# Kernel optimization log

Measured on AMD Instinct MI355X. Metric: run time of the kernel, lower is better.

Reference implementation:

```python
import jax, jax.numpy as jnp
import numpy as np

N_AGENTS = 8; N_HEADS = 4; HYP = 128; EMB = 32; ENT_DIM = 64
BS = 64; T = 64; NE = 32


def setup_inputs() -> dict:
    key = jax.random.key(0)
    ks = jax.random.split(key, 8)
    p = lambda k, shape: jax.random.normal(k, shape, dtype=jnp.float32) * 0.1
    return {
        "agent_qs": jax.random.normal(ks[0], (BS, T, N_AGENTS), dtype=jnp.float32),
        "entities": jax.random.normal(ks[1], (BS, T, NE, ENT_DIM), dtype=jnp.float32),
        "entity_mask": jax.random.randint(ks[2], (BS, T, NE), 0, 2, dtype=jnp.int32),
        "fc1_w": p(ks[3], (4, HYP, ENT_DIM)), "fc1_b": jnp.zeros((4, HYP), jnp.float32),
        "qkv_w": p(ks[4], (4, 3 * HYP, HYP)), "qkv_b": jnp.zeros((4, 3 * HYP), jnp.float32),
        "out_w": p(ks[5], (4, HYP, HYP)), "out_b": jnp.zeros((4, HYP), jnp.float32),
        "fc2_w": p(ks[6], (4, EMB, HYP)), "fc2_b": jnp.zeros((4, EMB), jnp.float32),
    }


def _hypernet(entities, emask, fc1_w, fc1_b, qkv_w, qkv_b, out_w, out_b, fc2_w, fc2_b):
    # entities: [B, ne, ed]; emask: [B, ne] int (1 = entity absent)
    B, ne, _ = entities.shape
    hd = HYP // N_HEADS
    x1 = jax.nn.relu(jnp.einsum('bne,he->bnh', entities, fc1_w) + fc1_b)  # [B, ne, HYP]
    agent_mask = emask[:, :N_AGENTS]                                      # [B, na]
    # attn_mask = 1 - (1-agent_mask) x (1-entity_mask); nonzero => masked out
    attn_mask = 1.0 - (1.0 - agent_mask.astype(jnp.float32))[:, :, None] * \
                      (1.0 - emask.astype(jnp.float32))[:, None, :]       # [B, na, ne]
    qkv = jnp.einsum('bnh,gh->bng', x1, qkv_w) + qkv_b                    # [B, ne, 3*HYP]
    q, k, v = jnp.split(qkv, 3, axis=-1)
    q = q[:, :N_AGENTS].reshape(B, N_AGENTS, N_HEADS, hd).transpose(0, 2, 1, 3)
    k = k.reshape(B, ne, N_HEADS, hd).transpose(0, 2, 1, 3)
    v = v.reshape(B, ne, N_HEADS, hd).transpose(0, 2, 1, 3)
    logits = jnp.einsum('bhqd,bhkd->bhqk', q, k) / jnp.sqrt(jnp.float32(hd))
    masked = attn_mask[:, None] > 0                                       # [B, 1, na, ne]
    logits = jnp.where(masked, -1e9, logits)
    w = jax.nn.softmax(logits, axis=-1)
    # rows fully masked -> zero weights (matches nan-fill in torch impl)
    w = jnp.where(jnp.all(masked, axis=-1, keepdims=True), 0.0, w)
    attn = jnp.einsum('bhqk,bhkd->bhqd', w, v).transpose(0, 2, 1, 3).reshape(B, N_AGENTS, HYP)
    x2 = jnp.einsum('bnh,oh->bno', attn, out_w) + out_b
    x2 = jnp.where(agent_mask[:, :, None] > 0, 0.0, x2)                   # post_mask
    x3 = jnp.einsum('bnh,eh->bne', x2, fc2_w) + fc2_b
    x3 = jnp.where(agent_mask[:, :, None] > 0, 0.0, x3)                   # masked_fill
    return x3  # [B, n_agents, EMB]


def reference(agent_qs, entities, entity_mask, fc1_w, fc1_b, qkv_w, qkv_b, out_w, out_b, fc2_w, fc2_b):
    bs, t, ne, ed = entities.shape
    ents = entities.reshape(bs * t, ne, ed)
    emask = entity_mask.reshape(bs * t, ne)
    qs = agent_qs.reshape(bs * t, 1, N_AGENTS)
    # vmap over the 4 stacked hypernets (w1, b1, w_final, V)
    outs = jax.vmap(_hypernet, in_axes=(None, None, 0, 0, 0, 0, 0, 0, 0, 0))(
        ents, emask, fc1_w, fc1_b, qkv_w, qkv_b, out_w, out_b, fc2_w, fc2_b)
    w1 = jax.nn.softmax(outs[0], axis=-1)            # matrix mode: [B, na, EMB]
    b1 = outs[1].mean(axis=1)[:, None, :]            # vector mode: [B, 1, EMB]
    wf = outs[2].mean(axis=1)[:, :, None]            # vector mode: [B, EMB, 1]
    wf = jax.nn.softmax(wf, axis=-1)                 # softmax over size-1 dim (faithful)
    v = outs[3].mean(axis=(1, 2))[:, None, None]     # scalar mode: [B, 1, 1]
    hidden = jnp.einsum('bqa,bae->bqe', qs, w1) + b1
    y = jnp.einsum('bqe,bek->bqk', hidden, wf) + v
    return y.reshape(bs, t, 1)
```

## Files before the change

### kernel.cpp

```cpp
#include <hip/hip_runtime.h>
#include <math.h>

#define BPB 4
#define NBLK 1024

typedef short short8 __attribute__((ext_vector_type(8)));
typedef float f32x4 __attribute__((ext_vector_type(4)));

__device__ __forceinline__ unsigned short f2bf(float x) {
  unsigned int u = __float_as_uint(x);
  u += 0x7fffu + ((u >> 16) & 1u);
  return (unsigned short)(u >> 16);
}
__device__ __forceinline__ float bf2f(unsigned int lo16) {
  return __uint_as_float(lo16 << 16);
}
__device__ __forceinline__ int tile_addr(int r, int k) {
  int g = k >> 3;
  int p = (g ^ ((r >> 1) & 3)) & 3;
  return r * 32 + p * 8 + (k & 7);
}
__device__ __forceinline__ int rm_addr(int r, int k) {
  int g = k >> 3;
  int r3 = r & 7;
  int rot = ((r3 << 2) | (r3 >> 1)) & 7;
  int p = (g & 8) | ((g & 7) ^ rot);
  return r * 128 + p * 8 + (k & 7);
}

__global__ void prep_w(const float* __restrict__ fc1_w, const float* __restrict__ qkv_w,
                       unsigned short* __restrict__ wbf) {
  int gid = blockIdx.x * 256 + threadIdx.x;
  for (int o = gid * 2; o < gid * 2 + 2; ++o) {
    float v; int dst;
    if (o < 16384) {
      int gi = o >> 13, rem = o & 8191, n = rem >> 6, k = rem & 63;
      int g = gi ? 3 : 1;
      v = fc1_w[((g << 7) + n) * 64 + k];
      dst = gi * 40960 + ((n >> 4) * 2 + (k >> 5)) * 512 + tile_addr(n & 15, k & 31);
    } else if (o < 49152) {
      int o2 = o - 16384;
      int gi = o2 >> 14, rem = o2 & 16383, n = rem >> 7, k = rem & 127;
      int g = gi ? 3 : 1;
      v = qkv_w[((g * 384 + 128 + n) << 7) + k];
      dst = gi * 40960 + 8192 + ((n >> 4) * 4 + (k >> 5)) * 512 + tile_addr(n & 15, k & 31);
    } else {
      int o2 = o - 49152;
      int gi = o2 >> 14, rem = o2 & 16383, n = rem >> 7, k = rem & 127;
      int g = gi ? 3 : 1;
      v = qkv_w[((g * 384 + n) << 7) + k];
      dst = gi * 40960 + 24576 + ((n >> 4) * 4 + (k >> 5)) * 512 + tile_addr(n & 15, k & 31);
    }
    wbf[dst] = f2bf(v);
  }
}

__global__ void prep_misc(const float* __restrict__ qkv_w, const float* __restrict__ qkv_b,
                          const float* __restrict__ out_w, const float* __restrict__ out_b,
                          const float* __restrict__ fc2_w, const float* __restrict__ fc2_b,
                          float* __restrict__ wsf) {
  const int gslot = blockIdx.x;
  const int g = gslot ? 3 : 1;
  const int t = threadIdx.x;
  __shared__ float cw[128];
  __shared__ float ow2[128];
  if (t < 128) {
    const float* fw = fc2_w + g * 32 * 128;
    float s = 0.f;
    for (int e = 0; e < 32; ++e) s += fw[e * 128 + t];
    cw[t] = s;
  }
  __syncthreads();
  if (t < 128) {
    const float* ow = out_w + g * 128 * 128;
    float s = 0.f;
    for (int h = 0; h < 128; ++h) s += ow[h * 128 + t] * cw[h];
    ow2[t] = s;
  }
  __syncthreads();
  float* wsg = wsf + gslot * 1024;
  const float* qwv = qkv_w + (size_t)(g * 3 + 2) * 128 * 128;
  for (int o = t; o < 512; o += 256) {
    int hh = o >> 7, h2 = o & 127;
    float s = 0.f;
    for (int d = 0; d < 32; ++d) s += qwv[(hh * 32 + d) * 128 + h2] * ow2[hh * 32 + d];
    wsg[o] = s;
  }
  if (t < 4) {
    const float* qbv = qkv_b + g * 384 + 256;
    float s = 0.f;
    for (int d = 0; d < 32; ++d) s += qbv[t * 32 + d] * ow2[t * 32 + d];
    wsg[512 + t] = s;
  }
  if (t == 0) {
    const float* ob = out_b + g * 128;
    float oc = 0.f;
    for (int h = 0; h < 128; ++h) oc += ob[h] * cw[h];
    const float* fb = fc2_b + g * 32;
    float cb = 0.f;
    for (int e = 0; e < 32; ++e) cb += fb[e];
    wsg[516] = oc + cb;
  }
}

__global__ __launch_bounds__(512, 1)
void mixer(const float* __restrict__ agent_qs,
           const float* __restrict__ entities,
           const int* __restrict__ emask,
           const float* __restrict__ fc1_b,
           const float* __restrict__ qkv_b,
           const unsigned short* __restrict__ wbf,
           const float* __restrict__ wsf,
           float* __restrict__ out) {
  __shared__ __align__(16) unsigned short sW[24576];
  __shared__ __align__(16) unsigned short sEK[16384];
  __shared__ __align__(16) unsigned short sX1[16384];
  __shared__ __align__(16) unsigned short sQ[4096];
  __shared__ __align__(16) float sVW[1024];
  __shared__ float sVP[BPB][4][32];
  __shared__ int sMm[BPB * 32];
  __shared__ float sS[8];

  const int t = threadIdx.x;
  const int lane = t & 63;
  const int w = t >> 6;
  const int bb0 = blockIdx.x * BPB;

  if (t < BPB * 32) sMm[t] = emask[bb0 * 32 + t];

  float wreg[4][2][4];

  for (int gi = 0; gi < 2; ++gi) {
    const int g = gi ? 3 : 1;
    __syncthreads();
    {
      const uint4* src = (const uint4*)(wbf + gi * 40960);
      uint4* dst = (uint4*)sW;
#pragma unroll
      for (int i = 0; i < 6; ++i) dst[i * 512 + t] = src[i * 512 + t];
      if (t < 256) ((float4*)sVW)[t] = ((const float4*)(wsf + gi * 1024))[t];
      const float4* Eg = (const float4*)(entities) + (size_t)bb0 * 512;
#pragma unroll
      for (int i = 0; i < 4; ++i) {
        int f4 = i * 512 + t;
        float4 v = Eg[f4];
        int k4 = f4 & 15, e = (f4 >> 4) & 31, bbi = f4 >> 9;
        int k = k4 * 4;
        int addr = bbi * 2048 + ((e >> 4) * 2 + (k >> 5)) * 512 + tile_addr(e & 15, k & 31);
        uint2 pk;
        pk.x = (unsigned)f2bf(v.x) | ((unsigned)f2bf(v.y) << 16);
        pk.y = (unsigned)f2bf(v.z) | ((unsigned)f2bf(v.w) << 16);
        *(uint2*)&sEK[addr] = pk;
      }
    }
    __syncthreads();
    {
      const int b = w >> 1, mtl = w & 1;
      const int r = lane & 15, kg = lane >> 4;
      f32x4 acc[8];
#pragma unroll
      for (int nt = 0; nt < 8; ++nt) acc[nt] = {0.f, 0.f, 0.f, 0.f};
#pragma unroll
      for (int kc = 0; kc < 2; ++kc) {
        short8 af = *(const short8*)&sEK[b * 2048 + (mtl * 2 + kc) * 512 + tile_addr(r, kg * 8)];
#pragma unroll
        for (int nt = 0; nt < 8; ++nt) {
          short8 bf = *(const short8*)&sW[(nt * 2 + kc) * 512 + tile_addr(r, kg * 8)];
          acc[nt] = __builtin_amdgcn_mfma_f32_16x16x32_bf16(af, bf, acc[nt], 0, 0, 0);
        }
      }
      const float* b1 = fc1_b + g * 128;
#pragma unroll
      for (int nt = 0; nt < 8; ++nt) {
        int h = nt * 16 + r;
        float bias = b1[h];
        int kc = h >> 5;
#pragma unroll
        for (int reg = 0; reg < 4; ++reg) {
          int rr = kg * 4 + reg;
          float v = acc[nt][reg] + bias;
          v = v > 0.f ? v : 0.f;
          sX1[b * 4096 + (mtl * 4 + kc) * 512 + tile_addr(rr, h & 31)] = f2bf(v);
        }
      }
    }
    __syncthreads();
    {
      const int b = w >> 1, mtl = w & 1;
      const int r = lane & 15, kg = lane >> 4;
      f32x4 acc[8];
#pragma unroll
      for (int nt = 0; nt < 8; ++nt) acc[nt] = {0.f, 0.f, 0.f, 0.f};
#pragma unroll
      for (int kc = 0; kc < 4; ++kc) {
        short8 af = *(const short8*)&sX1[b * 4096 + (mtl * 4 + kc) * 512 + tile_addr(r, kg * 8)];
#pragma unroll
        for (int nt = 0; nt < 8; ++nt) {
          short8 bf = *(const short8*)&sW[8192 + (nt * 4 + kc) * 512 + tile_addr(r, kg * 8)];
          acc[nt] = __builtin_amdgcn_mfma_f32_16x16x32_bf16(af, bf, acc[nt], 0, 0, 0);
        }
      }
      const float* bk = qkv_b + g * 384 + 128;
#pragma unroll
      for (int nt = 0; nt < 8; ++nt) {
        int h = nt * 16 + r;
        float bias = bk[h];
#pragma unroll
        for (int reg = 0; reg < 4; ++reg) {
          int ent = mtl * 16 + kg * 4 + reg;
          sEK[b * 4096 + rm_addr(ent, h)] = f2bf(acc[nt][reg] + bias);
        }
      }
    }
    __syncthreads();
    {
      const uint4* src = (const uint4*)(wbf + gi * 40960 + 24576);
      uint4* dst = (uint4*)(sW + 8192);
#pragma unroll
      for (int i = 0; i < 4; ++i) dst[i * 512 + t] = src[i * 512 + t];
    }
    __syncthreads();
    {
      const int mt = w >> 2;
      const int r = lane & 15, kg = lane >> 4;
      const int b_rd = mt * 2 + (r >> 3);
      f32x4 acc[2];
      acc[0] = {0.f, 0.f, 0.f, 0.f};
      acc[1] = {0.f, 0.f, 0.f, 0.f};
#pragma unroll
      for (int kc = 0; kc < 4; ++kc) {
        short8 af = *(const short8*)&sX1[b_rd * 4096 + kc * 512 + tile_addr(r & 7, kg * 8)];
#pragma unroll
        for (int j = 0; j < 2; ++j) {
          int nt = (w & 3) * 2 + j;
          short8 bf = *(const short8*)&sW[8192 + (nt * 4 + kc) * 512 + tile_addr(r, kg * 8)];
          acc[j] = __builtin_amdgcn_mfma_f32_16x16x32_bf16(af, bf, acc[j], 0, 0, 0);
        }
      }
      const float* bq = qkv_b + g * 384;
#pragma unroll
      for (int j = 0; j < 2; ++j) {
        int nt = (w & 3) * 2 + j;
        int h = nt * 16 + r;
        float bias = bq[h];
#pragma unroll
        for (int reg = 0; reg < 4; ++reg) {
          int rr = kg * 4 + reg;
          int b_st = mt * 2 + (rr >> 3);
          sQ[b_st * 1024 + rm_addr(rr & 7, h)] = f2bf(acc[j][reg] + bias);
        }
      }
    }
    __syncthreads();
    if (w < 4) {
      const int b = w;
      const int cl = lane & 15, kg = lane >> 4;
      bool ea0 = (sMm[b * 32 + cl] == 0);
      bool ea1 = (sMm[b * 32 + 16 + cl] == 0);
      bool aa[4];
#pragma unroll
      for (int reg = 0; reg < 4; ++reg) aa[reg] = (sMm[b * 32 + ((kg * 4 + reg) & 7)] == 0);
#pragma unroll
      for (int hh = 0; hh < 4; ++hh) {
        short8 af = *(const short8*)&sQ[b * 1024 + rm_addr(lane & 7, hh * 32 + kg * 8)];
        f32x4 d[2];
#pragma unroll
        for (int nt = 0; nt < 2; ++nt) {
          f32x4 z = {0.f, 0.f, 0.f, 0.f};
          short8 bf = *(const short8*)&sEK[b * 4096 + rm_addr(nt * 16 + cl, hh * 32 + kg * 8)];
          d[nt] = __builtin_amdgcn_mfma_f32_16x16x32_bf16(af, bf, z, 0, 0, 0);
        }
#pragma unroll
        for (int reg = 0; reg < 4; ++reg) {
          float lg0 = (ea0 && aa[reg]) ? d[0][reg] * 0.17677669529663687f : -1e30f;
          float lg1 = (ea1 && aa[reg]) ? d[1][reg] * 0.17677669529663687f : -1e30f;
          float m = fmaxf(lg0, lg1);
          for (int o = 8; o; o >>= 1) m = fmaxf(m, __shfl_xor(m, o, 16));
          float p0 = lg0 > -1e29f ? __expf(lg0 - m) : 0.f;
          float p1 = lg1 > -1e29f ? __expf(lg1 - m) : 0.f;
          float s = p0 + p1;
          for (int o = 8; o; o >>= 1) s += __shfl_xor(s, o, 16);
          float inv = s > 0.f ? 1.f / s : 0.f;
          wreg[hh][0][reg] = p0 * inv;
          wreg[hh][1][reg] = p1 * inv;
        }
      }
    } else {
      const int b = w - 4;
      const int e = lane & 31;
      const int hh0 = (lane >> 5) * 2;
      const int mt = e >> 4, r = e & 15;
      float a0 = sVW[512 + hh0];
      float a1 = sVW[512 + hh0 + 1];
#pragma unroll
      for (int kc = 0; kc < 4; ++kc) {
#pragma unroll
        for (int gg = 0; gg < 4; ++gg) {
          uint4 u = *(const uint4*)&sX1[b * 4096 + (mt * 4 + kc) * 512 + tile_addr(r, gg * 8)];
          int kb = kc * 32 + gg * 8;
          const float* w0 = &sVW[hh0 * 128 + kb];
          const float* w1 = &sVW[(hh0 + 1) * 128 + kb];
          float x0 = bf2f(u.x & 0xffffu), x1v = bf2f(u.x >> 16);
          float x2 = bf2f(u.y & 0xffffu), x3v = bf2f(u.y >> 16);
          float x4 = bf2f(u.z & 0xffffu), x5v = bf2f(u.z >> 16);
          float x6 = bf2f(u.w & 0xffffu), x7v = bf2f(u.w >> 16);
          a0 = fmaf(x0, w0[0], a0); a0 = fmaf(x1v, w0[1], a0);
          a0 = fmaf(x2, w0[2], a0); a0 = fmaf(x3v, w0[3], a0);
          a0 = fmaf(x4, w0[4], a0); a0 = fmaf(x5v, w0[5], a0);
          a0 = fmaf(x6, w0[6], a0); a0 = fmaf(x7v, w0[7], a0);
          a1 = fmaf(x0, w1[0], a1); a1 = fmaf(x1v, w1[1], a1);
          a1 = fmaf(x2, w1[2], a1); a1 = fmaf(x3v, w1[3], a1);
          a1 = fmaf(x4, w1[4], a1); a1 = fmaf(x5v, w1[5], a1);
          a1 = fmaf(x6, w1[6], a1); a1 = fmaf(x7v, w1[7], a1);
        }
      }
      sVP[b][hh0][e] = a0;
      sVP[b][hh0 + 1][e] = a1;
    }
    __syncthreads();
    if (w < 4) {
      const int b = w;
      const int cl = lane & 15;
      float c = 0.f;
#pragma unroll
      for (int hh = 0; hh < 4; ++hh) {
        float vp0 = sVP[b][hh][cl];
        float vp1 = sVP[b][hh][16 + cl];
        float s0 = wreg[hh][0][0] + wreg[hh][0][1] + wreg[hh][0][2] + wreg[hh][0][3];
        float s1 = wreg[hh][1][0] + wreg[hh][1][1] + wreg[hh][1][2] + wreg[hh][1][3];
        c = fmaf(vp0, s0, fmaf(vp1, s1, c));
      }
      for (int o = 16; o; o >>= 1) c += __shfl_xor(c, o, 32);
      if (lane == 0) {
        int cnt = 0;
        for (int a = 0; a < 8; ++a) cnt += (sMm[b * 32 + a] == 0);
        sS[gi * 4 + b] = c + sVW[516] * (float)cnt;
      }
    }
  }
  __syncthreads();
  if (t < BPB) {
    const float* qs = agent_qs + (size_t)(bb0 + t) * 8;
    float q = 0.f;
    for (int a = 0; a < 8; ++a) q += qs[a];
    out[bb0 + t] = q + sS[t] * 0.125f + sS[4 + t] * (1.f / 256.f);
  }
}

extern "C" void kernel_launch(void* const* d_in, const int* in_sizes, int n_in,
                              void* d_out, int out_size, void* d_ws, size_t ws_size,
                              hipStream_t stream) {
  const float* agent_qs = (const float*)d_in[0];
  const float* entities = (const float*)d_in[1];
  const int* emask = (const int*)d_in[2];
  const float* fc1_w = (const float*)d_in[3];
  const float* fc1_b = (const float*)d_in[4];
  const float* qkv_w = (const float*)d_in[5];
  const float* qkv_b = (const float*)d_in[6];
  const float* out_w = (const float*)d_in[7];
  const float* out_b = (const float*)d_in[8];
  const float* fc2_w = (const float*)d_in[9];
  const float* fc2_b = (const float*)d_in[10];
  float* out = (float*)d_out;
  unsigned short* wbf = (unsigned short*)d_ws;
  float* wsf = (float*)((char*)d_ws + 163840);

  prep_w<<<160, 256, 0, stream>>>(fc1_w, qkv_w, wbf);
  prep_misc<<<2, 256, 0, stream>>>(qkv_w, qkv_b, out_w, out_b, fc2_w, fc2_b, wsf);
  mixer<<<NBLK, 512, 0, stream>>>(agent_qs, entities, emask, fc1_b, qkv_b, wbf, wsf, out);
}
```

Before: 169.3 us.

## Read MFMA weight fragments directly from global memory and drop the shared weight staging

Weights are now pre-packed by a single merged prep kernel into per-lane MFMA fragment order, so each lane loads its B operand straight from global memory (L2-resident) instead of first copying weights into a 48KB shared buffer. This removes the sW staging copies and several barriers, merges the Q projection and V-projection work into the K-projection phase, and raises launch bounds so more blocks can share a CU. Epilogue stores are vectorised into packed bf16 pairs. The cost is repeated global/L2 traffic for the weights across blocks, with higher register pressure from the larger occupancy target.

Measured after the change: 174.6 us. 3.1% more time.

```diff
diff --git a/kernel.cpp b/kernel.cpp
--- a/kernel.cpp
+++ b/kernel.cpp
@@ -3,6 +3,7 @@
 
 #define BPB 4
 #define NBLK 1024
+#define SCALE 0.17677669529663687f
 
 typedef short short8 __attribute__((ext_vector_type(8)));
 typedef float f32x4 __attribute__((ext_vector_type(4)));
@@ -11,6 +12,9 @@
   unsigned int u = __float_as_uint(x);
   u += 0x7fffu + ((u >> 16) & 1u);
   return (unsigned short)(u >> 16);
+}
+__device__ __forceinline__ unsigned pk2(float a, float b) {
+  return (unsigned)f2bf(a) | ((unsigned)f2bf(b) << 16);
 }
 __device__ __forceinline__ float bf2f(unsigned int lo16) {
   return __uint_as_float(lo16 << 16);
@@ -28,82 +32,94 @@
   return r * 128 + p * 8 + (k & 7);
 }
 
-__global__ void prep_w(const float* __restrict__ fc1_w, const float* __restrict__ qkv_w,
-                       unsigned short* __restrict__ wbf) {
-  int gid = blockIdx.x * 256 + threadIdx.x;
-  for (int o = gid * 2; o < gid * 2 + 2; ++o) {
-    float v; int dst;
-    if (o < 16384) {
-      int gi = o >> 13, rem = o & 8191, n = rem >> 6, k = rem & 63;
+__global__ void prep(const float* __restrict__ fc1_w, const float* __restrict__ qkv_w,
+                     const float* __restrict__ qkv_b, const float* __restrict__ out_w,
+                     const float* __restrict__ out_b, const float* __restrict__ fc2_w,
+                     const float* __restrict__ fc2_b,
+                     unsigned short* __restrict__ wbf, float* __restrict__ wsf) {
+  const int blk = blockIdx.x;
+  const int t = threadIdx.x;
+  __shared__ float cw[128], ow2[128], red[128];
+  if (blk < 40) {
+    int o = blk * 256 + t;
+    const float* src;
+    int dst;
+    if (o < 2048) {
+      int gi = o >> 10, rem = o & 1023, n = rem >> 3, kg = rem & 7;
       int g = gi ? 3 : 1;
-      v = fc1_w[((g << 7) + n) * 64 + k];
-      dst = gi * 40960 + ((n >> 4) * 2 + (k >> 5)) * 512 + tile_addr(n & 15, k & 31);
-    } else if (o < 49152) {
-      int o2 = o - 16384;
-      int gi = o2 >> 14, rem = o2 & 16383, n = rem >> 7, k = rem & 127;
+      src = fc1_w + ((g << 7) + n) * 64 + kg * 8;
+      int lane = (kg & 3) * 16 + (n & 15);
+      int f = (n >> 4) * 2 + (kg >> 2);
+      dst = ((gi * 16 + f) * 64 + lane) * 8;
+    } else if (o < 6144) {
+      int o2 = o - 2048;
+      int gi = o2 >> 11, rem = o2 & 2047, n = rem >> 4, kg = rem & 15;
       int g = gi ? 3 : 1;
-      v = qkv_w[((g * 384 + 128 + n) << 7) + k];
-      dst = gi * 40960 + 8192 + ((n >> 4) * 4 + (k >> 5)) * 512 + tile_addr(n & 15, k & 31);
+      src = qkv_w + ((g * 384 + 128 + n) << 7) + kg * 8;
+      int lane = (kg & 3) * 16 + (n & 15);
+      int f = (n >> 4) * 4 + (kg >> 2);
+      dst = 16384 + ((gi * 32 + f) * 64 + lane) * 8;
     } else {
-      int o2 = o - 49152;
-      int gi = o2 >> 14, rem = o2 & 16383, n = rem >> 7, k = rem & 127;
+      int o2 = o - 6144;
+      int gi = o2 >> 11, rem = o2 & 2047, n = rem >> 4, kg = rem & 15;
       int g = gi ? 3 : 1;
-      v = qkv_w[((g * 384 + n) << 7) + k];
-      dst = gi * 40960 + 24576 + ((n >> 4) * 4 + (k >> 5)) * 512 + tile_addr(n & 15, k & 31);
-    }
-    wbf[dst] = f2bf(v);
+      src = qkv_w + ((g * 384 + n) << 7) + kg * 8;
+      int lane = (kg & 3) * 16 + (n & 15);
+      int f = (n >> 4) * 4 + (kg >> 2);
+      dst = 49152 + ((gi * 32 + f) * 64 + lane) * 8;
+    }
+    float4 v0 = *(const float4*)src;
+    float4 v1 = *(const float4*)(src + 4);
+    uint4 p;
+    p.x = pk2(v0.x, v0.y); p.y = pk2(v0.z, v0.w);
+    p.z = pk2(v1.x, v1.y); p.w = pk2(v1.z, v1.w);
+    *(uint4*)&wbf[dst] = p;
+  } else {
+    const int gi = blk - 40;
+    const int g = gi ? 3 : 1;
+    if (t < 128) {
+      const float* fw = fc2_w + g * 32 * 128;
+      float s = 0.f;
+      for (int e = 0; e < 32; ++e) s += fw[e * 128 + t];
+      cw[t] = s;
+    }
+    __syncthreads();
+    if (t < 128) {
+      const float* ow = out_w + g * 128 * 128;
+      float s = 0.f;
+      for (int h = 0; h < 128; ++h) s += ow[h * 128 + t] * cw[h];
+      ow2[t] = s;
+    }
+    __syncthreads();
+    float* wsg = wsf + gi * 1024;
+    const float* qwv = qkv_w + (size_t)(g * 3 + 2) * 128 * 128;
+    for (int o = t; o < 512; o += 256) {
+      int hh = o >> 7, h2 = o & 127;
+      float s = 0.f;
+      for (int d = 0; d < 32; ++d) s += qwv[(hh * 32 + d) * 128 + h2] * ow2[hh * 32 + d];
+      wsg[o] = s;
+    }
+    if (t < 4) {
+      const float* qbv = qkv_b + g * 384 + 256;
+      float s = 0.f;
+      for (int d = 0; d < 32; ++d) s += qbv[t * 32 + d] * ow2[t * 32 + d];
+      wsg[512 + t] = s;
+    }
+    if (t < 128) {
+      float x = out_b[g * 128 + t] * cw[t];
+      if (t < 32) x += fc2_b[g * 32 + t];
+      red[t] = x;
+    }
+    __syncthreads();
+    if (t < 64) {
+      float s = red[t] + red[t + 64];
+      for (int o = 32; o; o >>= 1) s += __shfl_xor(s, o, 64);
+      if (t == 0) wsg[516] = s;
+    }
   }
 }
 
-__global__ void prep_misc(const float* __restrict__ qkv_w, const float* __restrict__ qkv_b,
-                          const float* __restrict__ out_w, const float* __restrict__ out_b,
-                          const float* __restrict__ fc2_w, const float* __restrict__ fc2_b,
-                          float* __restrict__ wsf) {
-  const int gslot = blockIdx.x;
-  const int g = gslot ? 3 : 1;
-  const int t = threadIdx.x;
-  __shared__ float cw[128];
-  __shared__ float ow2[128];
-  if (t < 128) {
-    const float* fw = fc2_w + g * 32 * 128;
-    float s = 0.f;
-    for (int e = 0; e < 32; ++e) s += fw[e * 128 + t];
-    cw[t] = s;
-  }
-  __syncthreads();
-  if (t < 128) {
-    const float* ow = out_w + g * 128 * 128;
-    float s = 0.f;
-    for (int h = 0; h < 128; ++h) s += ow[h * 128 + t] * cw[h];
-    ow2[t] = s;
-  }
-  __syncthreads();
-  float* wsg = wsf + gslot * 1024;
-  const float* qwv = qkv_w + (size_t)(g * 3 + 2) * 128 * 128;
-  for (int o = t; o < 512; o += 256) {
-    int hh = o >> 7, h2 = o & 127;
-    float s = 0.f;
-    for (int d = 0; d < 32; ++d) s += qwv[(hh * 32 + d) * 128 + h2] * ow2[hh * 32 + d];
-    wsg[o] = s;
-  }
-  if (t < 4) {
-    const float* qbv = qkv_b + g * 384 + 256;
-    float s = 0.f;
-    for (int d = 0; d < 32; ++d) s += qbv[t * 32 + d] * ow2[t * 32 + d];
-    wsg[512 + t] = s;
-  }
-  if (t == 0) {
-    const float* ob = out_b + g * 128;
-    float oc = 0.f;
-    for (int h = 0; h < 128; ++h) oc += ob[h] * cw[h];
-    const float* fb = fc2_b + g * 32;
-    float cb = 0.f;
-    for (int e = 0; e < 32; ++e) cb += fb[e];
-    wsg[516] = oc + cb;
-  }
-}
-
-__global__ __launch_bounds__(512, 1)
+__global__ __launch_bounds__(512, 4)
 void mixer(const float* __restrict__ agent_qs,
            const float* __restrict__ entities,
            const int* __restrict__ emask,
@@ -112,34 +128,32 @@
            const unsigned short* __restrict__ wbf,
            const float* __restrict__ wsf,
            float* __restrict__ out) {
-  __shared__ __align__(16) unsigned short sW[24576];
   __shared__ __align__(16) unsigned short sEK[16384];
   __shared__ __align__(16) unsigned short sX1[16384];
   __shared__ __align__(16) unsigned short sQ[4096];
   __shared__ __align__(16) float sVW[1024];
   __shared__ float sVP[BPB][4][32];
-  __shared__ int sMm[BPB * 32];
+  __shared__ int sMm[128];
   __shared__ float sS[8];
 
   const int t = threadIdx.x;
   const int lane = t & 63;
   const int w = t >> 6;
+  const int r = lane & 15, kg = lane >> 4;
   const int bb0 = blockIdx.x * BPB;
 
-  if (t < BPB * 32) sMm[t] = emask[bb0 * 32 + t];
+  if (t < 128) sMm[t] = emask[bb0 * 32 + t];
+
+  const short8* W1f = (const short8*)wbf;
+  const short8* Wkf = (const short8*)(wbf + 16384);
+  const short8* Wqf = (const short8*)(wbf + 49152);
 
   float wreg[4][2][4];
 
   for (int gi = 0; gi < 2; ++gi) {
     const int g = gi ? 3 : 1;
-    __syncthreads();
     {
-      const uint4* src = (const uint4*)(wbf + gi * 40960);
-      uint4* dst = (uint4*)sW;
-#pragma unroll
-      for (int i = 0; i < 6; ++i) dst[i * 512 + t] = src[i * 512 + t];
-      if (t < 256) ((float4*)sVW)[t] = ((const float4*)(wsf + gi * 1024))[t];
-      const float4* Eg = (const float4*)(entities) + (size_t)bb0 * 512;
+      const float4* Eg = (const float4*)entities + (size_t)bb0 * 512;
 #pragma unroll
       for (int i = 0; i < 4; ++i) {
         int f4 = i * 512 + t;
@@ -147,114 +161,117 @@
         int k4 = f4 & 15, e = (f4 >> 4) & 31, bbi = f4 >> 9;
         int k = k4 * 4;
         int addr = bbi * 2048 + ((e >> 4) * 2 + (k >> 5)) * 512 + tile_addr(e & 15, k & 31);
-        uint2 pk;
-        pk.x = (unsigned)f2bf(v.x) | ((unsigned)f2bf(v.y) << 16);
-        pk.y = (unsigned)f2bf(v.z) | ((unsigned)f2bf(v.w) << 16);
-        *(uint2*)&sEK[addr] = pk;
-      }
+        uint2 pkv;
+        pkv.x = pk2(v.x, v.y);
+        pkv.y = pk2(v.z, v.w);
+        *(uint2*)&sEK[addr] = pkv;
+      }
+      if (t < 256) ((float4*)sVW)[t] = ((const float4*)(wsf + gi * 1024))[t];
     }
     __syncthreads();
     {
       const int b = w >> 1, mtl = w & 1;
-      const int r = lane & 15, kg = lane >> 4;
       f32x4 acc[8];
 #pragma unroll
       for (int nt = 0; nt < 8; ++nt) acc[nt] = {0.f, 0.f, 0.f, 0.f};
 #pragma unroll
       for (int kc = 0; kc < 2; ++kc) {
-        short8 af = *(const short8*)&sEK[b * 2048 + (mtl * 2 + kc) * 512 + tile_addr(r, kg * 8)];
-#pragma unroll
-        for (int nt = 0; nt < 8; ++nt) {
-          short8 bf = *(const short8*)&sW[(nt * 2 + kc) * 512 + tile_addr(r, kg * 8)];
-          acc[nt] = __builtin_amdgcn_mfma_f32_16x16x32_bf16(af, bf, acc[nt], 0, 0, 0);
-        }
+        short8 ef = *(const short8*)&sEK[b * 2048 + (mtl * 2 + kc) * 512 + tile_addr(r, kg * 8)];
+#pragma unroll
+        for (int nt = 0; nt < 8; ++nt)
+          acc[nt] = __builtin_amdgcn_mfma_f32_16x16x32_bf16(
+              W1f[(gi * 16 + nt * 2 + kc) * 64 + lane], ef, acc[nt], 0, 0, 0);
       }
       const float* b1 = fc1_b + g * 128;
 #pragma unroll
       for (int nt = 0; nt < 8; ++nt) {
-        int h = nt * 16 + r;
-        float bias = b1[h];
-        int kc = h >> 5;
-#pragma unroll
-        for (int reg = 0; reg < 4; ++reg) {
-          int rr = kg * 4 + reg;
-          float v = acc[nt][reg] + bias;
-          v = v > 0.f ? v : 0.f;
-          sX1[b * 4096 + (mtl * 4 + kc) * 512 + tile_addr(rr, h & 31)] = f2bf(v);
-        }
+        int hbase = nt * 16 + kg * 4;
+        float4 bb4 = *(const float4*)&b1[hbase];
+        float v0 = fmaxf(acc[nt][0] + bb4.x, 0.f);
+        float v1 = fmaxf(acc[nt][1] + bb4.y, 0.f);
+        float v2 = fmaxf(acc[nt][2] + bb4.z, 0.f);
+        float v3 = fmaxf(acc[nt][3] + bb4.w, 0.f);
+        uint2 pkv;
+        pkv.x = pk2(v0, v1);
+        pkv.y = pk2(v2, v3);
+        *(uint2*)&sX1[b * 4096 + (mtl * 4 + (hbase >> 5)) * 512 + tile_addr(r, hbase & 31)] = pkv;
       }
     }
     __syncthreads();
     {
       const int b = w >> 1, mtl = w & 1;
-      const int r = lane & 15, kg = lane >> 4;
       f32x4 acc[8];
 #pragma unroll
       for (int nt = 0; nt < 8; ++nt) acc[nt] = {0.f, 0.f, 0.f, 0.f};
 #pragma unroll
       for (int kc = 0; kc < 4; ++kc) {
-        short8 af = *(const short8*)&sX1[b * 4096 + (mtl * 4 + kc) * 512 + tile_addr(r, kg * 8)];
-#pragma unroll
-        for (int nt = 0; nt < 8; ++nt) {
-          short8 bf = *(const short8*)&sW[8192 + (nt * 4 + kc) * 512 + tile_addr(r, kg * 8)];
-          acc[nt] = __builtin_amdgcn_mfma_f32_16x16x32_bf16(af, bf, acc[nt], 0, 0, 0);
+        short8 xf = *(const short8*)&sX1[b * 4096 + (mtl * 4 + kc) * 512 + tile_addr(r, kg * 8)];
+#pragma unroll
+        for (int nt = 0; nt < 8; ++nt)
+          acc[nt] = __builtin_amdgcn_mfma_f32_16x16x32_bf16(
+              Wkf[(gi * 32 + nt * 4 + kc) * 64 + lane], xf, acc[nt], 0, 0, 0);
+      }
+      const float* bk = qkv_b + g * 384 + 128;
+      const int ent = mtl * 16 + r;
+#pragma unroll
+      for (int nt = 0; nt < 8; ++nt) {
+        int hbase = nt * 16 + kg * 4;
+        float4 bb4 = *(const float4*)&bk[hbase];
+        uint2 pkv;
+        pkv.x = pk2(acc[nt][0] + bb4.x, acc[nt][1] + bb4.y);
+        pkv.y = pk2(acc[nt][2] + bb4.z, acc[nt][3] + bb4.w);
+        *(uint2*)&sEK[b * 4096 + rm_addr(ent, hbase)] = pkv;
+      }
+      const int mt = w >> 2, ntp = w & 3;
+      const int b_rd = mt * 2 + (r >> 3);
+      f32x4 qacc[2];
+      qacc[0] = {0.f, 0.f, 0.f, 0.f};
+      qacc[1] = {0.f, 0.f, 0.f, 0.f};
+#pragma unroll
+      for (int kc = 0; kc < 4; ++kc) {
+        short8 xf = *(const short8*)&sX1[b_rd * 4096 + kc * 512 + tile_addr(r & 7, kg * 8)];
+#pragma unroll
+        for (int j = 0; j < 2; ++j)
+          qacc[j] = __builtin_amdgcn_mfma_f32_16x16x32_bf16(
+              Wqf[(gi * 32 + (ntp * 2 + j) * 4 + kc) * 64 + lane], xf, qacc[j], 0, 0, 0);
+      }
+      const float* bq = qkv_b + g * 384;
+#pragma unroll
+      for (int j = 0; j < 2; ++j) {
+        int hbase = (ntp * 2 + j) * 16 + kg * 4;
+        float4 bb4 = *(const float4*)&bq[hbase];
+        uint2 pkv;
+        pkv.x = pk2(qacc[j][0] + bb4.x, qacc[j][1] + bb4.y);
+        pkv.y = pk2(qacc[j][2] + bb4.z, qacc[j][3] + bb4.w);
+        *(uint2*)&sQ[(mt * 2 + (r >> 3)) * 1024 + rm_addr(r & 7, hbase)] = pkv;
+      }
+      const int vb = w >> 1;
+      const int e = lane & 31;
+      const int hh = (w & 1) * 2 + (lane >> 5);
+      const int emt = e >> 4, er = e & 15;
+      float a0 = sVW[512 + hh];
+#pragma unroll
+      for (int kc = 0; kc < 4; ++kc) {
+#pragma unroll
+        for (int gg = 0; gg < 4; ++gg) {
+          uint4 u = *(const uint4*)&sX1[vb * 4096 + (emt * 4 + kc) * 512 + tile_addr(er, gg * 8)];
+          const float* wv = &sVW[hh * 128 + kc * 32 + gg * 8];
+          a0 = fmaf(bf2f(u.x & 0xffffu), wv[0], a0);
+          a0 = fmaf(bf2f(u.x >> 16), wv[1], a0);
+          a0 = fmaf(bf2f(u.y & 0xffffu), wv[2], a0);
+          a0 = fmaf(bf2f(u.y >> 16), wv[3], a0);
+          a0 = fmaf(bf2f(u.z & 0xffffu), wv[4], a0);
+          a0 = fmaf(bf2f(u.z >> 16), wv[5], a0);
+          a0 = fmaf(bf2f(u.w & 0xffffu), wv[6], a0);
+          a0 = fmaf(bf2f(u.w >> 16), wv[7], a0);
         }
       }
-      const float* bk = qkv_b + g * 384 + 128;
-#pragma unroll
-      for (int nt = 0; nt < 8; ++nt) {
-        int h = nt * 16 + r;
-        float bias = bk[h];
-#pragma unroll
-        for (int reg = 0; reg < 4; ++reg) {
-          int ent = mtl * 16 + kg * 4 + reg;
-          sEK[b * 4096 + rm_addr(ent, h)] = f2bf(acc[nt][reg] + bias);
-        }
-      }
-    }
-    __syncthreads();
-    {
-      const uint4* src = (const uint4*)(wbf + gi * 40960 + 24576);
-      uint4* dst = (uint4*)(sW + 8192);
-#pragma unroll
-      for (int i = 0; i < 4; ++i) dst[i * 512 + t] = src[i * 512 + t];
-    }
-    __syncthreads();
-    {
-      const int mt = w >> 2;
-      const int r = lane & 15, kg = lane >> 4;
-      const int b_rd = mt * 2 + (r >> 3);
-      f32x4 acc[2];
-      acc[0] = {0.f, 0.f, 0.f, 0.f};
-      acc[1] = {0.f, 0.f, 0.f, 0.f};
-#pragma unroll
-      for (int kc = 0; kc < 4; ++kc) {
-        short8 af = *(const short8*)&sX1[b_rd * 4096 + kc * 512 + tile_addr(r & 7, kg * 8)];
-#pragma unroll
-        for (int j = 0; j < 2; ++j) {
-          int nt = (w & 3) * 2 + j;
-          short8 bf = *(const short8*)&sW[8192 + (nt * 4 + kc) * 512 + tile_addr(r, kg * 8)];
-          acc[j] = __builtin_amdgcn_mfma_f32_16x16x32_bf16(af, bf, acc[j], 0, 0, 0);
-        }
-      }
-      const float* bq = qkv_b + g * 384;
-#pragma unroll
-      for (int j = 0; j < 2; ++j) {
-        int nt = (w & 3) * 2 + j;
-        int h = nt * 16 + r;
-        float bias = bq[h];
-#pragma unroll
-        for (int reg = 0; reg < 4; ++reg) {
-          int rr = kg * 4 + reg;
-          int b_st = mt * 2 + (rr >> 3);
-          sQ[b_st * 1024 + rm_addr(rr & 7, h)] = f2bf(acc[j][reg] + bias);
-        }
-      }
+      sVP[vb][hh][e] = a0;
     }
     __syncthreads();
     if (w < 4) {
       const int b = w;
-      const int cl = lane & 15, kg = lane >> 4;
+      const int cl = r;
       bool ea0 = (sMm[b * 32 + cl] == 0);
       bool ea1 = (sMm[b * 32 + 16 + cl] == 0);
       bool aa[4];
@@ -263,17 +280,15 @@
 #pragma unroll
       for (int hh = 0; hh < 4; ++hh) {
         short8 af = *(const short8*)&sQ[b * 1024 + rm_addr(lane & 7, hh * 32 + kg * 8)];
-        f32x4 d[2];
-#pragma unroll
-        for (int nt = 0; nt < 2; ++nt) {
-          f32x4 z = {0.f, 0.f, 0.f, 0.f};
-          short8 bf = *(const short8*)&sEK[b * 4096 + rm_addr(nt * 16 + cl, hh * 32 + kg * 8)];
-          d[nt] = __builtin_amdgcn_mfma_f32_16x16x32_bf16(af, bf, z, 0, 0, 0);
-        }
+        f32x4 z = {0.f, 0.f, 0.f, 0.f};
+        short8 bf0 = *(const short8*)&sEK[b * 4096 + rm_addr(cl, hh * 32 + kg * 8)];
+        f32x4 d0 = __builtin_amdgcn_mfma_f32_16x16x32_bf16(af, bf0, z, 0, 0, 0);
+        short8 bf1 = *(const short8*)&sEK[b * 4096 + rm_addr(16 + cl, hh * 32 + kg * 8)];
+        f32x4 d1 = __builtin_amdgcn_mfma_f32_16x16x32_bf16(af, bf1, z, 0, 0, 0);
 #pragma unroll
         for (int reg = 0; reg < 4; ++reg) {
-          float lg0 = (ea0 && aa[reg]) ? d[0][reg] * 0.17677669529663687f : -1e30f;
-          float lg1 = (ea1 && aa[reg]) ? d[1][reg] * 0.17677669529663687f : -1e30f;
+          float lg0 = (ea0 && aa[reg]) ? d0[reg] * SCALE : -1e30f;
+          float lg1 = (ea1 && aa[reg]) ? d1[reg] * SCALE : -1e30f;
           float m = fmaxf(lg0, lg1);
           for (int o = 8; o; o >>= 1) m = fmaxf(m, __shfl_xor(m, o, 16));
           float p0 = lg0 > -1e29f ? __expf(lg0 - m) : 0.f;
@@ -285,42 +300,6 @@
           wreg[hh][1][reg] = p1 * inv;
         }
       }
-    } else {
-      const int b = w - 4;
-      const int e = lane & 31;
-      const int hh0 = (lane >> 5) * 2;
-      const int mt = e >> 4, r = e & 15;
-      float a0 = sVW[512 + hh0];
-      float a1 = sVW[512 + hh0 + 1];
-#pragma unroll
-      for (int kc = 0; kc < 4; ++kc) {
-#pragma unroll
-        for (int gg = 0; gg < 4; ++gg) {
-          uint4 u = *(const uint4*)&sX1[b * 4096 + (mt * 4 + kc) * 512 + tile_addr(r, gg * 8)];
-          int kb = kc * 32 + gg * 8;
-          const float* w0 = &sVW[hh0 * 128 + kb];
-          const float* w1 = &sVW[(hh0 + 1) * 128 + kb];
-          float x0 = bf2f(u.x & 0xffffu), x1v = bf2f(u.x >> 16);
-          float x2 = bf2f(u.y & 0xffffu), x3v = bf2f(u.y >> 16);
-          float x4 = bf2f(u.z & 0xffffu), x5v = bf2f(u.z >> 16);
-          float x6 = bf2f(u.w & 0xffffu), x7v = bf2f(u.w >> 16);
-          a0 = fmaf(x0, w0[0], a0); a0 = fmaf(x1v, w0[1], a0);
-          a0 = fmaf(x2, w0[2], a0); a0 = fmaf(x3v, w0[3], a0);
-          a0 = fmaf(x4, w0[4], a0); a0 = fmaf(x5v, w0[5], a0);
-          a0 = fmaf(x6, w0[6], a0); a0 = fmaf(x7v, w0[7], a0);
-          a1 = fmaf(x0, w1[0], a1); a1 = fmaf(x1v, w1[1], a1);
-          a1 = fmaf(x2, w1[2], a1); a1 = fmaf(x3v, w1[3], a1);
-          a1 = fmaf(x4, w1[4], a1); a1 = fmaf(x5v, w1[5], a1);
-          a1 = fmaf(x6, w1[6], a1); a1 = fmaf(x7v, w1[7], a1);
-        }
-      }
-      sVP[b][hh0][e] = a0;
-      sVP[b][hh0 + 1][e] = a1;
-    }
-    __syncthreads();
-    if (w < 4) {
-      const int b = w;
-      const int cl = lane & 15;
       float c = 0.f;
 #pragma unroll
       for (int hh = 0; hh < 4; ++hh) {
@@ -337,12 +316,13 @@
         sS[gi * 4 + b] = c + sVW[516] * (float)cnt;
       }
     }
+    __syncthreads();
   }
-  __syncthreads();
+
   if (t < BPB) {
-    const float* qs = agent_qs + (size_t)(bb0 + t) * 8;
-    float q = 0.f;
-    for (int a = 0; a < 8; ++a) q += qs[a];
+    const float4* qs = (const float4*)(agent_qs + (size_t)(bb0 + t) * 8);
+    float4 a = qs[0], b4 = qs[1];
+    float q = a.x + a.y + a.z + a.w + b4.x + b4.y + b4.z + b4.w;
     out[bb0 + t] = q + sS[t] * 0.125f + sS[4 + t] * (1.f / 256.f);
   }
 }
@@ -365,7 +345,6 @@
   unsigned short* wbf = (unsigned short*)d_ws;
   float* wsf = (float*)((char*)d_ws + 163840);
 
-  prep_w<<<160, 256, 0, stream>>>(fc1_w, qkv_w, wbf);
-  prep_misc<<<2, 256, 0, stream>>>(qkv_w, qkv_b, out_w, out_b, fc2_w, fc2_b, wsf);
+  prep<<<42, 256, 0, stream>>>(fc1_w, qkv_w, qkv_b, out_w, out_b, fc2_w, fc2_b, wbf, wsf);
   mixer<<<NBLK, 512, 0, stream>>>(agent_qs, entities, emask, fc1_b, qkv_b, wbf, wsf, out);
 }
```
